# Kernel tuning notes

Hardware: AMD Instinct MI355X
Metric: run time of the kernel (lower is better)

The kernel has to match this reference:

```python
import jax, jax.numpy as jnp
import numpy as np

H = 8  # num_heads

def setup_inputs() -> dict:
    key = jax.random.key(0)
    k1, k2, k3, k4 = jax.random.split(key, 4)
    B, T, D, K = 16, 8192, 512, 4
    x = jax.random.normal(k1, (B, T, D), dtype=jnp.float32)
    mask = jax.random.randint(k2, (B, T), 0, 2, dtype=jnp.int32)
    queries = jax.random.normal(k3, (1, K, D), dtype=jnp.float32) * 0.02
    # xavier_uniform for (D, D) Linear weight
    limit = np.sqrt(6.0 / (D + D))
    w_out = jax.random.uniform(k4, (D, D), dtype=jnp.float32, minval=-limit, maxval=limit)
    b_out = jnp.zeros((D,), dtype=jnp.float32)
    return {"x": x, "mask": mask, "queries": queries, "w_out": w_out, "b_out": b_out}

def reference(x, mask, queries, w_out, b_out):
    B, T, D = x.shape
    K = queries.shape[1]
    hd = D // H
    scale = jnp.sqrt(jnp.float32(hd))
    q = queries.reshape(K, H, hd)          # shared across batch
    kv = x.reshape(B, T, H, hd)            # keys == values
    scores = jnp.einsum('khd,bthd->bhkt', q, kv) / scale  # (B,H,K,T)
    scores = jnp.where(mask[:, None, None, :] == 0, jnp.float32(-1e9), scores)
    attn = jax.nn.softmax(scores, axis=-1)  # dropout is identity in eval / p=0
    out = jnp.einsum('bhkt,bthd->bkhd', attn, kv).reshape(B, K, D)
    return out @ w_out.T + b_out
```

## Files before the change

### kernel.cpp

```cpp
#include <hip/hip_runtime.h>
#include <math.h>

#define BB 16
#define TT 8192
#define DD 512
#define KK 4
#define HH 8
#define HD 64

__global__ __launch_bounds__(256, 2)
void attn_partial_kernel(const float* __restrict__ x,
                         const int* __restrict__ mask,
                         const float* __restrict__ queries,
                         float* __restrict__ ws,
                         int NC) {
    const int C     = TT / NC;
    const int iters = C >> 1;
    const int b     = blockIdx.x / NC;
    const int c     = blockIdx.x % NC;
    const int t0    = c * C;
    const int tid   = threadIdx.x;
    const int slot  = tid >> 7;
    const int lane  = tid & 127;
    const int h     = lane >> 4;
    const int g     = lane & 15;

    __shared__ int   smask[8192];
    __shared__ float smerge[128 * 20];

    for (int i = tid; i < C; i += 256) smask[i] = mask[b * TT + t0 + i];
    __syncthreads();

    const float4* q4 = reinterpret_cast<const float4*>(queries);
    float4 q0 = q4[0 * 128 + lane];
    float4 q1 = q4[1 * 128 + lane];
    float4 q2 = q4[2 * 128 + lane];
    float4 q3 = q4[3 * 128 + lane];
    const float sc = 0.125f;
    q0.x *= sc; q0.y *= sc; q0.z *= sc; q0.w *= sc;
    q1.x *= sc; q1.y *= sc; q1.z *= sc; q1.w *= sc;
    q2.x *= sc; q2.y *= sc; q2.z *= sc; q2.w *= sc;
    q3.x *= sc; q3.y *= sc; q3.z *= sc; q3.w *= sc;

    float4 acc0 = {0.f, 0.f, 0.f, 0.f};
    float4 acc1 = {0.f, 0.f, 0.f, 0.f};
    float4 acc2 = {0.f, 0.f, 0.f, 0.f};
    float4 acc3 = {0.f, 0.f, 0.f, 0.f};
    float l0 = 0.f, l1 = 0.f, l2 = 0.f, l3 = 0.f;

    const float4* xp = reinterpret_cast<const float4*>(x) +
                       ((size_t)(b * TT + t0 + slot)) * 128 + lane;

    float4 xv = *xp;
    int    mv = smask[slot];

    for (int i = 0; i < iters; ++i) {
        float4 xc = xv;
        int    mc = mv;
        if (i + 1 < iters) {
            xp += 256;
            xv = *xp;
            mv = smask[2 * (i + 1) + slot];
        }

        float s0 = fmaf(q0.x, xc.x, fmaf(q0.y, xc.y, fmaf(q0.z, xc.z, q0.w * xc.w)));
        float s1 = fmaf(q1.x, xc.x, fmaf(q1.y, xc.y, fmaf(q1.z, xc.z, q1.w * xc.w)));
        float s2 = fmaf(q2.x, xc.x, fmaf(q2.y, xc.y, fmaf(q2.z, xc.z, q2.w * xc.w)));
        float s3 = fmaf(q3.x, xc.x, fmaf(q3.y, xc.y, fmaf(q3.z, xc.z, q3.w * xc.w)));

        #pragma unroll
        for (int off = 1; off <= 8; off <<= 1) {
            s0 += __shfl_xor(s0, off);
            s1 += __shfl_xor(s1, off);
            s2 += __shfl_xor(s2, off);
            s3 += __shfl_xor(s3, off);
        }

        const float w0 = mc ? __expf(s0) : 0.f;
        const float w1 = mc ? __expf(s1) : 0.f;
        const float w2 = mc ? __expf(s2) : 0.f;
        const float w3 = mc ? __expf(s3) : 0.f;

        l0 += w0; l1 += w1; l2 += w2; l3 += w3;
        acc0.x = fmaf(w0, xc.x, acc0.x); acc0.y = fmaf(w0, xc.y, acc0.y);
        acc0.z = fmaf(w0, xc.z, acc0.z); acc0.w = fmaf(w0, xc.w, acc0.w);
        acc1.x = fmaf(w1, xc.x, acc1.x); acc1.y = fmaf(w1, xc.y, acc1.y);
        acc1.z = fmaf(w1, xc.z, acc1.z); acc1.w = fmaf(w1, xc.w, acc1.w);
        acc2.x = fmaf(w2, xc.x, acc2.x); acc2.y = fmaf(w2, xc.y, acc2.y);
        acc2.z = fmaf(w2, xc.z, acc2.z); acc2.w = fmaf(w2, xc.w, acc2.w);
        acc3.x = fmaf(w3, xc.x, acc3.x); acc3.y = fmaf(w3, xc.y, acc3.y);
        acc3.z = fmaf(w3, xc.z, acc3.z); acc3.w = fmaf(w3, xc.w, acc3.w);
    }

    if (slot == 1) {
        float* p = &smerge[lane * 20];
        p[0]  = acc0.x; p[1]  = acc0.y; p[2]  = acc0.z; p[3]  = acc0.w;
        p[4]  = acc1.x; p[5]  = acc1.y; p[6]  = acc1.z; p[7]  = acc1.w;
        p[8]  = acc2.x; p[9]  = acc2.y; p[10] = acc2.z; p[11] = acc2.w;
        p[12] = acc3.x; p[13] = acc3.y; p[14] = acc3.z; p[15] = acc3.w;
        p[16] = l0; p[17] = l1; p[18] = l2; p[19] = l3;
    }
    __syncthreads();
    if (slot == 0) {
        const float* p = &smerge[lane * 20];
        acc0.x += p[0];  acc0.y += p[1];  acc0.z += p[2];  acc0.w += p[3];
        acc1.x += p[4];  acc1.y += p[5];  acc1.z += p[6];  acc1.w += p[7];
        acc2.x += p[8];  acc2.y += p[9];  acc2.z += p[10]; acc2.w += p[11];
        acc3.x += p[12]; acc3.y += p[13]; acc3.z += p[14]; acc3.w += p[15];
        l0 += p[16]; l1 += p[17]; l2 += p[18]; l3 += p[19];

        float4* O4 = reinterpret_cast<float4*>(ws);
        const size_t o16 = ((((size_t)b * NC + c) * HH + h) * KK) * 16 + g;
        O4[o16 + 0 * 16] = acc0;
        O4[o16 + 1 * 16] = acc1;
        O4[o16 + 2 * 16] = acc2;
        O4[o16 + 3 * 16] = acc3;
        if (g == 0) {
            float* lp = ws + (size_t)BB * NC * HH * KK * 64;
            const size_t li = (((size_t)b * NC + c) * HH + h) * KK;
            lp[li + 0] = l0; lp[li + 1] = l1; lp[li + 2] = l2; lp[li + 3] = l3;
        }
    }
}

__global__ __launch_bounds__(256, 4)
void merge_gemm_kernel(const float* __restrict__ ws,
                       const float* __restrict__ w_out,
                       const float* __restrict__ b_out,
                       float* __restrict__ out,
                       int NC) {
    const int bk  = blockIdx.x;
    const int b   = bk >> 2;
    const int k   = bk & 3;
    const int tid = threadIdx.x;

    __shared__ __align__(16) float row[512];
    __shared__ float linv[8];

    if (tid < 8) {
        const float* lp = ws + (size_t)BB * NC * HH * KK * 64;
        float s = 0.f;
        for (int c = 0; c < NC; ++c)
            s += lp[(((size_t)b * NC + c) * HH + tid) * KK + k];
        linv[tid] = 1.0f / s;
    }
    __syncthreads();

    for (int item = tid; item < 512; item += 256) {
        const int h = item >> 6, d = item & 63;
        float s = 0.f;
        for (int c = 0; c < NC; ++c)
            s += ws[((((size_t)b * NC + c) * HH + h) * KK + k) * 64 + d];
        row[item] = s * linv[h];
    }
    __syncthreads();

    const float4* W4 = reinterpret_cast<const float4*>(w_out);
    const float4* R4 = reinterpret_cast<const float4*>(row);
    float a0 = b_out[tid];
    float a1 = b_out[tid + 256];
    for (int d4 = 0; d4 < 128; ++d4) {
        const float4 r  = R4[d4];
        const float4 wa = W4[(size_t)tid * 128 + d4];
        const float4 wb = W4[((size_t)tid + 256) * 128 + d4];
        a0 = fmaf(r.x, wa.x, fmaf(r.y, wa.y, fmaf(r.z, wa.z, fmaf(r.w, wa.w, a0))));
        a1 = fmaf(r.x, wb.x, fmaf(r.y, wb.y, fmaf(r.z, wb.z, fmaf(r.w, wb.w, a1))));
    }
    out[(size_t)bk * 512 + tid]       = a0;
    out[(size_t)bk * 512 + tid + 256] = a1;
}

extern "C" void kernel_launch(void* const* d_in, const int* in_sizes, int n_in,
                              void* d_out, int out_size, void* d_ws, size_t ws_size,
                              hipStream_t stream) {
    const float* x       = (const float*)d_in[0];
    const int*   mask    = (const int*)d_in[1];
    const float* queries = (const float*)d_in[2];
    const float* w_out   = (const float*)d_in[3];
    const float* b_out   = (const float*)d_in[4];
    float*       out     = (float*)d_out;
    float*       ws      = (float*)d_ws;

    int NC = 32;
    while (NC > 1 && (size_t)BB * NC * HH * KK * 65 * 4 > ws_size) NC >>= 1;

    attn_partial_kernel<<<BB * NC, 256, 0, stream>>>(x, mask, queries, ws, NC);
    merge_gemm_kernel<<<BB * KK, 256, 0, stream>>>(ws, w_out, b_out, out, NC);
}
```

Measured before the change: 428.6 us.

## Process 8 tokens per block with 16 dims per thread and wider loads

Restructures the partial attention kernel so each 32-thread group handles one token, with each thread covering 16 contiguous dims (four float4 loads) instead of 4. The score reduction needs only 2 shuffle steps instead of 4, and 8 token slots run in parallel instead of 2, giving more loads in flight per block. The cost is more registers per thread (64 accumulators plus 64 query values), which may hurt occupancy under launch_bounds(256,2), and a larger shared-memory merge across 8 slots. The NC fallback floor is raised to 16 so smask[512] always fits the chunk size.

```diff
diff --git a/kernel.cpp b/kernel.cpp
--- a/kernel.cpp
+++ b/kernel.cpp
@@ -15,111 +15,124 @@
                          float* __restrict__ ws,
                          int NC) {
     const int C     = TT / NC;
-    const int iters = C >> 1;
+    const int iters = C >> 3;
     const int b     = blockIdx.x / NC;
     const int c     = blockIdx.x % NC;
     const int t0    = c * C;
     const int tid   = threadIdx.x;
-    const int slot  = tid >> 7;
-    const int lane  = tid & 127;
-    const int h     = lane >> 4;
-    const int g     = lane & 15;
-
-    __shared__ int   smask[8192];
-    __shared__ float smerge[128 * 20];
+    const int slot  = tid >> 5;
+    const int seg   = tid & 31;
+    const int h     = seg >> 2;
+    const int qd    = seg & 3;
+
+    __shared__ int    smask[512];
+    __shared__ float4 smerge[8 * 512];
+    __shared__ float  smerge_l[8 * 32];
 
     for (int i = tid; i < C; i += 256) smask[i] = mask[b * TT + t0 + i];
     __syncthreads();
 
     const float4* q4 = reinterpret_cast<const float4*>(queries);
-    float4 q0 = q4[0 * 128 + lane];
-    float4 q1 = q4[1 * 128 + lane];
-    float4 q2 = q4[2 * 128 + lane];
-    float4 q3 = q4[3 * 128 + lane];
-    const float sc = 0.125f;
-    q0.x *= sc; q0.y *= sc; q0.z *= sc; q0.w *= sc;
-    q1.x *= sc; q1.y *= sc; q1.z *= sc; q1.w *= sc;
-    q2.x *= sc; q2.y *= sc; q2.z *= sc; q2.w *= sc;
-    q3.x *= sc; q3.y *= sc; q3.z *= sc; q3.w *= sc;
-
-    float4 acc0 = {0.f, 0.f, 0.f, 0.f};
-    float4 acc1 = {0.f, 0.f, 0.f, 0.f};
-    float4 acc2 = {0.f, 0.f, 0.f, 0.f};
-    float4 acc3 = {0.f, 0.f, 0.f, 0.f};
-    float l0 = 0.f, l1 = 0.f, l2 = 0.f, l3 = 0.f;
+    float4 qv[4][4];
+    #pragma unroll
+    for (int k = 0; k < 4; ++k)
+        #pragma unroll
+        for (int j = 0; j < 4; ++j) {
+            float4 v = q4[k * 128 + seg * 4 + j];
+            v.x *= 0.125f; v.y *= 0.125f; v.z *= 0.125f; v.w *= 0.125f;
+            qv[k][j] = v;
+        }
+
+    float4 av[4][4];
+    #pragma unroll
+    for (int k = 0; k < 4; ++k)
+        #pragma unroll
+        for (int j = 0; j < 4; ++j) av[k][j] = make_float4(0.f, 0.f, 0.f, 0.f);
+    float l[4] = {0.f, 0.f, 0.f, 0.f};
 
     const float4* xp = reinterpret_cast<const float4*>(x) +
-                       ((size_t)(b * TT + t0 + slot)) * 128 + lane;
-
-    float4 xv = *xp;
-    int    mv = smask[slot];
+                       ((size_t)(b * TT + t0 + slot)) * 128 + seg * 4;
+
+    float4 pf[4];
+    #pragma unroll
+    for (int j = 0; j < 4; ++j) pf[j] = xp[j];
+    int mv = smask[slot];
 
     for (int i = 0; i < iters; ++i) {
-        float4 xc = xv;
-        int    mc = mv;
+        float4 xc[4];
+        #pragma unroll
+        for (int j = 0; j < 4; ++j) xc[j] = pf[j];
+        const int mc = mv;
         if (i + 1 < iters) {
-            xp += 256;
-            xv = *xp;
-            mv = smask[2 * (i + 1) + slot];
-        }
-
-        float s0 = fmaf(q0.x, xc.x, fmaf(q0.y, xc.y, fmaf(q0.z, xc.z, q0.w * xc.w)));
-        float s1 = fmaf(q1.x, xc.x, fmaf(q1.y, xc.y, fmaf(q1.z, xc.z, q1.w * xc.w)));
-        float s2 = fmaf(q2.x, xc.x, fmaf(q2.y, xc.y, fmaf(q2.z, xc.z, q2.w * xc.w)));
-        float s3 = fmaf(q3.x, xc.x, fmaf(q3.y, xc.y, fmaf(q3.z, xc.z, q3.w * xc.w)));
-
-        #pragma unroll
-        for (int off = 1; off <= 8; off <<= 1) {
-            s0 += __shfl_xor(s0, off);
-            s1 += __shfl_xor(s1, off);
-            s2 += __shfl_xor(s2, off);
-            s3 += __shfl_xor(s3, off);
-        }
-
-        const float w0 = mc ? __expf(s0) : 0.f;
-        const float w1 = mc ? __expf(s1) : 0.f;
-        const float w2 = mc ? __expf(s2) : 0.f;
-        const float w3 = mc ? __expf(s3) : 0.f;
-
-        l0 += w0; l1 += w1; l2 += w2; l3 += w3;
-        acc0.x = fmaf(w0, xc.x, acc0.x); acc0.y = fmaf(w0, xc.y, acc0.y);
-        acc0.z = fmaf(w0, xc.z, acc0.z); acc0.w = fmaf(w0, xc.w, acc0.w);
-        acc1.x = fmaf(w1, xc.x, acc1.x); acc1.y = fmaf(w1, xc.y, acc1.y);
-        acc1.z = fmaf(w1, xc.z, acc1.z); acc1.w = fmaf(w1, xc.w, acc1.w);
-        acc2.x = fmaf(w2, xc.x, acc2.x); acc2.y = fmaf(w2, xc.y, acc2.y);
-        acc2.z = fmaf(w2, xc.z, acc2.z); acc2.w = fmaf(w2, xc.w, acc2.w);
-        acc3.x = fmaf(w3, xc.x, acc3.x); acc3.y = fmaf(w3, xc.y, acc3.y);
-        acc3.z = fmaf(w3, xc.z, acc3.z); acc3.w = fmaf(w3, xc.w, acc3.w);
-    }
-
-    if (slot == 1) {
-        float* p = &smerge[lane * 20];
-        p[0]  = acc0.x; p[1]  = acc0.y; p[2]  = acc0.z; p[3]  = acc0.w;
-        p[4]  = acc1.x; p[5]  = acc1.y; p[6]  = acc1.z; p[7]  = acc1.w;
-        p[8]  = acc2.x; p[9]  = acc2.y; p[10] = acc2.z; p[11] = acc2.w;
-        p[12] = acc3.x; p[13] = acc3.y; p[14] = acc3.z; p[15] = acc3.w;
-        p[16] = l0; p[17] = l1; p[18] = l2; p[19] = l3;
-    }
-    __syncthreads();
-    if (slot == 0) {
-        const float* p = &smerge[lane * 20];
-        acc0.x += p[0];  acc0.y += p[1];  acc0.z += p[2];  acc0.w += p[3];
-        acc1.x += p[4];  acc1.y += p[5];  acc1.z += p[6];  acc1.w += p[7];
-        acc2.x += p[8];  acc2.y += p[9];  acc2.z += p[10]; acc2.w += p[11];
-        acc3.x += p[12]; acc3.y += p[13]; acc3.z += p[14]; acc3.w += p[15];
-        l0 += p[16]; l1 += p[17]; l2 += p[18]; l3 += p[19];
-
-        float4* O4 = reinterpret_cast<float4*>(ws);
-        const size_t o16 = ((((size_t)b * NC + c) * HH + h) * KK) * 16 + g;
-        O4[o16 + 0 * 16] = acc0;
-        O4[o16 + 1 * 16] = acc1;
-        O4[o16 + 2 * 16] = acc2;
-        O4[o16 + 3 * 16] = acc3;
-        if (g == 0) {
-            float* lp = ws + (size_t)BB * NC * HH * KK * 64;
-            const size_t li = (((size_t)b * NC + c) * HH + h) * KK;
-            lp[li + 0] = l0; lp[li + 1] = l1; lp[li + 2] = l2; lp[li + 3] = l3;
-        }
+            xp += 1024;
+            #pragma unroll
+            for (int j = 0; j < 4; ++j) pf[j] = xp[j];
+            mv = smask[8 * (i + 1) + slot];
+        }
+
+        float s[4];
+        #pragma unroll
+        for (int k = 0; k < 4; ++k) {
+            float a = 0.f;
+            #pragma unroll
+            for (int j = 0; j < 4; ++j) {
+                a = fmaf(qv[k][j].x, xc[j].x, a);
+                a = fmaf(qv[k][j].y, xc[j].y, a);
+                a = fmaf(qv[k][j].z, xc[j].z, a);
+                a = fmaf(qv[k][j].w, xc[j].w, a);
+            }
+            s[k] = a;
+        }
+        #pragma unroll
+        for (int k = 0; k < 4; ++k) {
+            s[k] += __shfl_xor(s[k], 1);
+            s[k] += __shfl_xor(s[k], 2);
+        }
+
+        float w[4];
+        #pragma unroll
+        for (int k = 0; k < 4; ++k) w[k] = mc ? __expf(s[k]) : 0.f;
+        #pragma unroll
+        for (int k = 0; k < 4; ++k) {
+            l[k] += w[k];
+            #pragma unroll
+            for (int j = 0; j < 4; ++j) {
+                av[k][j].x = fmaf(w[k], xc[j].x, av[k][j].x);
+                av[k][j].y = fmaf(w[k], xc[j].y, av[k][j].y);
+                av[k][j].z = fmaf(w[k], xc[j].z, av[k][j].z);
+                av[k][j].w = fmaf(w[k], xc[j].w, av[k][j].w);
+            }
+        }
+    }
+
+    #pragma unroll
+    for (int k = 0; k < 4; ++k)
+        #pragma unroll
+        for (int j = 0; j < 4; ++j)
+            smerge[slot * 512 + (h * 4 + k) * 16 + qd * 4 + j] = av[k][j];
+    if (qd == 0) {
+        #pragma unroll
+        for (int k = 0; k < 4; ++k) smerge_l[slot * 32 + h * 4 + k] = l[k];
+    }
+    __syncthreads();
+
+    float4* O4 = reinterpret_cast<float4*>(ws);
+    const size_t obase = ((size_t)b * NC + c) * 512;
+    for (int f = tid; f < 512; f += 256) {
+        float4 sacc = smerge[f];
+        #pragma unroll
+        for (int s2 = 1; s2 < 8; ++s2) {
+            float4 v = smerge[s2 * 512 + f];
+            sacc.x += v.x; sacc.y += v.y; sacc.z += v.z; sacc.w += v.w;
+        }
+        O4[obase + f] = sacc;
+    }
+    if (tid < 32) {
+        float sacc = 0.f;
+        #pragma unroll
+        for (int s2 = 0; s2 < 8; ++s2) sacc += smerge_l[s2 * 32 + tid];
+        float* lp = ws + (size_t)BB * NC * HH * KK * 64;
+        lp[(((size_t)b * NC + c) * HH + (tid >> 2)) * KK + (tid & 3)] = sacc;
     }
 }
 
@@ -182,7 +195,7 @@
     float*       ws      = (float*)d_ws;
 
     int NC = 32;
-    while (NC > 1 && (size_t)BB * NC * HH * KK * 65 * 4 > ws_size) NC >>= 1;
+    while (NC > 16 && (size_t)BB * NC * HH * KK * 65 * 4 > ws_size) NC >>= 1;
 
     attn_partial_kernel<<<BB * NC, 256, 0, stream>>>(x, mask, queries, ws, NC);
     merge_gemm_kernel<<<BB * KK, 256, 0, stream>>>(ws, w_out, b_out, out, NC);
```

Measured after the change: 418.2 us. 2.4% less time.
